# Performance work log

Hardware: AMD Instinct MI355X
Metric: run time of the kernel (lower is better)

The kernel has to match this reference:

```python
import jax, jax.numpy as jnp
import numpy as np

INPUT_SIZE = 1024
HIDDEN_SIZE = 1024
BATCH = 4096


def setup_inputs() -> dict:
    key = jax.random.key(0)
    ks = jax.random.split(key, 20)
    k = 1.0 / HIDDEN_SIZE
    bound = float(np.sqrt(k))

    def u(kk, shape):
        return jax.random.uniform(kk, shape, jnp.float32, -bound, bound)

    inp = {
        "x": jax.random.normal(ks[0], (BATCH, INPUT_SIZE), jnp.float32),
        "h0": jax.random.normal(ks[1], (BATCH, HIDDEN_SIZE), jnp.float32),
        "c0": jax.random.normal(ks[2], (BATCH, HIDDEN_SIZE), jnp.float32),
        "W_ii": u(ks[3], (INPUT_SIZE, HIDDEN_SIZE)), "b_ii": u(ks[4], (HIDDEN_SIZE,)),
        "W_if": u(ks[5], (INPUT_SIZE, HIDDEN_SIZE)), "b_if": u(ks[6], (HIDDEN_SIZE,)),
        "W_ig": u(ks[7], (INPUT_SIZE, HIDDEN_SIZE)), "b_ig": u(ks[8], (HIDDEN_SIZE,)),
        "W_io": u(ks[9], (INPUT_SIZE, HIDDEN_SIZE)), "b_io": u(ks[10], (HIDDEN_SIZE,)),
        "W_hi": u(ks[11], (HIDDEN_SIZE, HIDDEN_SIZE)), "b_hi": u(ks[12], (HIDDEN_SIZE,)),
        "W_hf": u(ks[13], (HIDDEN_SIZE, HIDDEN_SIZE)), "b_hf": u(ks[14], (HIDDEN_SIZE,)),
        "W_hg": u(ks[15], (HIDDEN_SIZE, HIDDEN_SIZE)), "b_hg": u(ks[16], (HIDDEN_SIZE,)),
        "W_ho": u(ks[17], (HIDDEN_SIZE, HIDDEN_SIZE)), "b_ho": u(ks[18], (HIDDEN_SIZE,)),
    }
    return inp


def reference(x, h0, c0,
              W_ii, b_ii, W_if, b_if, W_ig, b_ig, W_io, b_io,
              W_hi, b_hi, W_hf, b_hf, W_hg, b_hg, W_ho, b_ho):
    # Fuse the 4 input-side and 4 hidden-side GEMMs into two wide GEMMs,
    # then a single fused gate computation — same math as the original.
    Wi = jnp.concatenate([W_ii, W_if, W_ig, W_io], axis=1)  # [In, 4H]
    Wh = jnp.concatenate([W_hi, W_hf, W_hg, W_ho], axis=1)  # [H, 4H]
    b = jnp.concatenate([b_ii + b_hi, b_if + b_hf, b_ig + b_hg, b_io + b_ho])
    gates = x @ Wi + h0 @ Wh + b  # [B, 4H]
    zi, zf, zg, zo = jnp.split(gates, 4, axis=1)
    i = jax.nn.sigmoid(zi)
    f = jax.nn.sigmoid(zf)
    g = jnp.tanh(zg)
    o = jax.nn.sigmoid(zo)
    c1 = f * c0 + i * g
    h1 = o * c1
    return h1, c1
```

## Files before the change

### kernel.cpp

```cpp
#include <hip/hip_runtime.h>

typedef unsigned short u16;
typedef unsigned int u32;
typedef __attribute__((ext_vector_type(8))) short short8;
typedef __attribute__((ext_vector_type(4))) float f32x4;

__device__ __forceinline__ u16 f2b(float f) {
  u32 u = __builtin_bit_cast(u32, f);
  u32 r = (u + 0x7FFFu + ((u >> 16) & 1u)) >> 16;
  return (u16)r;
}

__device__ __forceinline__ void gl_lds16(const void* g, void* l) {
  __builtin_amdgcn_global_load_lds(
      (const __attribute__((address_space(1))) u32*)g,
      (__attribute__((address_space(3))) u32*)l, 16, 0, 0);
}

struct Ptrs8 { const float* p[8]; };

__global__ __launch_bounds__(256) void wt_pack(Ptrs8 w, u16* __restrict__ Wt) {
  __shared__ float lds[64 * 64];
  const int tid = threadIdx.x;
  const int bid = blockIdx.x;
  const int mat = bid >> 8;
  const int g = mat & 3, h = mat >> 2;
  const int tile = bid & 255;
  const int kt = tile >> 4, nt = tile & 15;
  const float* __restrict__ src = w.p[mat];

#pragma unroll
  for (int i = 0; i < 4; ++i) {
    int c = tid + i * 256;
    int k = c >> 4, n4 = (c & 15) * 4;
    gl_lds16(src + (size_t)(kt * 64 + k) * 1024 + nt * 64 + n4, &lds[c * 4]);
  }
  asm volatile("s_waitcnt vmcnt(0)");
  __syncthreads();

#pragma unroll
  for (int i = 0; i < 2; ++i) {
    int c = tid + i * 256;
    int n = c & 63, kb = (c >> 6) * 8;
    short8 v;
#pragma unroll
    for (int j = 0; j < 8; ++j) v[j] = (short)f2b(lds[(kb + j) * 64 + n]);
    size_t off = (size_t)(g * 1024 + nt * 64 + n) * 2048 + h * 1024 + kt * 64 + kb;
    *reinterpret_cast<short8*>(Wt + off) = v;
  }
}

__global__ __launch_bounds__(256) void xh_pack(const float* __restrict__ x,
                                               const float* __restrict__ h0,
                                               u16* __restrict__ Ap) {
  int t = blockIdx.x * 256 + threadIdx.x;
  int m = t >> 8, kc = t & 255;
  const float* src = (kc < 128) ? (x + (size_t)m * 1024 + kc * 8)
                                : (h0 + (size_t)m * 1024 + (kc - 128) * 8);
  float4 a = *reinterpret_cast<const float4*>(src);
  float4 b = *reinterpret_cast<const float4*>(src + 4);
  short8 v;
  v[0] = (short)f2b(a.x); v[1] = (short)f2b(a.y);
  v[2] = (short)f2b(a.z); v[3] = (short)f2b(a.w);
  v[4] = (short)f2b(b.x); v[5] = (short)f2b(b.y);
  v[6] = (short)f2b(b.z); v[7] = (short)f2b(b.w);
  *reinterpret_cast<short8*>(Ap + (size_t)m * 2048 + kc * 8) = v;
}

__global__ void bias_pack(Ptrs8 b, float* __restrict__ bias) {
  int i = blockIdx.x * 1024 + threadIdx.x;
  int g = i >> 10, n = i & 1023;
  bias[i] = b.p[g][n] + b.p[4 + g][n];
}

#define LD8(base, off) (*reinterpret_cast<const short8*>((base) + (off)))
#define MFMA_(a, b, c) __builtin_amdgcn_mfma_f32_16x16x32_bf16(a, b, c, 0, 0, 0)

#define READ_A(DST, BASE)                                   \
  _Pragma("unroll")                                         \
  for (int mi = 0; mi < 4; ++mi) {                          \
    DST[mi][0] = LD8(Ab, arow + (BASE + mi) * 1024 + c0k);  \
    DST[mi][1] = LD8(Ab, arow + (BASE + mi) * 1024 + c1k);  \
  }
#define READ_B(DST, GB)                                     \
  _Pragma("unroll")                                         \
  for (int g = 0; g < 2; ++g) {                             \
    DST[g][0] = LD8(Bb, bbase + (GB + g) * 4096 + c0k);     \
    DST[g][1] = LD8(Bb, bbase + (GB + g) * 4096 + c1k);     \
  }
#define MFMA_QUAD(AF, BF, MO, GO)                                              \
  __builtin_amdgcn_s_setprio(1);                                               \
  _Pragma("unroll")                                                            \
  for (int mi = 0; mi < 4; ++mi)                                               \
    _Pragma("unroll")                                                          \
    for (int g = 0; g < 2; ++g) {                                              \
      acc[MO + mi][GO + g] = MFMA_(AF[mi][0], BF[g][0], acc[MO + mi][GO + g]); \
      acc[MO + mi][GO + g] = MFMA_(AF[mi][1], BF[g][1], acc[MO + mi][GO + g]); \
    }                                                                          \
  __builtin_amdgcn_s_setprio(0);

__global__ __launch_bounds__(512, 2) void lstm_fused(
    const u16* __restrict__ Ap, const float* __restrict__ c0,
    const u16* __restrict__ Wt, const float* __restrict__ bias,
    float* __restrict__ out) {
  __shared__ u16 As[2][256 * 64];
  __shared__ u16 Bs[2][256 * 64];

  const int tid = threadIdx.x;
  const int lane = tid & 63;
  const int wid = tid >> 6;
  const int wr = wid >> 2;
  const int wc = wid & 3;
  const int fl = lane & 15;
  const int hi = lane >> 4;
  const int lo7 = fl & 7;

  const int bid0 = blockIdx.x;
  const int sbid = (bid0 & 7) * 32 + (bid0 >> 3);
  const int m0 = (sbid >> 4) * 256;
  const int n0 = (sbid & 15) * 64;

  int aoff[4], boff[4];
#pragma unroll
  for (int i = 0; i < 4; ++i) {
    const int L = tid + i * 512;
    const int r = L >> 3, cL = L & 7;
    const int cg = cL ^ (r & 7);
    aoff[i] = (m0 + r) * 2048 + cg * 8;
    const int ge = r >> 6, wce = (r >> 4) & 3, ue = r & 15;
    boff[i] = (ge * 1024 + n0 + wce * 16 + ue) * 2048 + cg * 8;
  }

  auto stageA = [&](int buf, int t, int h) {
    const int k0 = t * 64;
    gl_lds16(Ap + aoff[h] + k0, &As[buf][(tid + h * 512) * 8]);
    gl_lds16(Ap + aoff[h + 2] + k0, &As[buf][(tid + (h + 2) * 512) * 8]);
  };
  auto stageB = [&](int buf, int t, int h) {
    const int k0 = t * 64;
    gl_lds16(Wt + boff[2 * h] + k0, &Bs[buf][(tid + (2 * h) * 512) * 8]);
    gl_lds16(Wt + boff[2 * h + 1] + k0, &Bs[buf][(tid + (2 * h + 1) * 512) * 8]);
  };

  const int c0k = (hi ^ lo7) * 8;
  const int c1k = ((4 + hi) ^ lo7) * 8;
  const int arow = (wr * 128 + fl) * 64;
  const int bbase = (wc * 16 + fl) * 64;

  f32x4 acc[8][4] = {};

  stageB(0, 0, 0);
  stageA(0, 0, 0);
  stageA(0, 0, 1);
  stageB(0, 0, 1);

  for (int t = 0; t < 31; ++t) {
    const int cur = t & 1, nxt = cur ^ 1;
    const u16* Ab = &As[cur][0];
    const u16* Bb = &Bs[cur][0];
    short8 af03[4][2], af47[4][2], bf01[2][2], bf23[2][2];

    asm volatile("s_waitcnt vmcnt(4)" ::: "memory");
    __builtin_amdgcn_s_barrier();
    READ_A(af03, 0)
    READ_B(bf01, 0)
    stageB(nxt, t + 1, 0);
    MFMA_QUAD(af03, bf01, 0, 0)

    asm volatile("s_waitcnt vmcnt(4)" ::: "memory");
    __builtin_amdgcn_s_barrier();
    READ_A(af47, 4)
    stageA(nxt, t + 1, 0);
    MFMA_QUAD(af47, bf01, 4, 0)

    asm volatile("s_waitcnt vmcnt(4)" ::: "memory");
    __builtin_amdgcn_s_barrier();
    READ_B(bf23, 2)
    stageA(nxt, t + 1, 1);
    MFMA_QUAD(af03, bf23, 0, 2)

    __builtin_amdgcn_s_barrier();
    stageB(nxt, t + 1, 1);
    MFMA_QUAD(af47, bf23, 4, 2)
  }

  {
    const u16* Ab = &As[1][0];
    const u16* Bb = &Bs[1][0];
    short8 af03[4][2], af47[4][2], bf01[2][2], bf23[2][2];

    asm volatile("s_waitcnt vmcnt(4)" ::: "memory");
    __builtin_amdgcn_s_barrier();
    READ_A(af03, 0)
    READ_B(bf01, 0)
    MFMA_QUAD(af03, bf01, 0, 0)

    asm volatile("s_waitcnt vmcnt(2)" ::: "memory");
    __builtin_amdgcn_s_barrier();
    READ_A(af47, 4)
    MFMA_QUAD(af47, bf01, 4, 0)

    asm volatile("s_waitcnt vmcnt(0)" ::: "memory");
    __builtin_amdgcn_s_barrier();
    READ_B(bf23, 2)
    MFMA_QUAD(af03, bf23, 0, 2)

    __builtin_amdgcn_s_barrier();
    MFMA_QUAD(af47, bf23, 4, 2)
  }

  const int col = n0 + wc * 16 + fl;
  float bv[4];
#pragma unroll
  for (int g = 0; g < 4; ++g) bv[g] = bias[g * 1024 + col];

#pragma unroll
  for (int mi = 0; mi < 8; ++mi) {
#pragma unroll
    for (int r = 0; r < 4; ++r) {
      const int row = m0 + wr * 128 + mi * 16 + hi * 4 + r;
      const float zi = acc[mi][0][r] + bv[0];
      const float zf = acc[mi][1][r] + bv[1];
      const float zg = acc[mi][2][r] + bv[2];
      const float zo = acc[mi][3][r] + bv[3];
      const float ig = 1.f / (1.f + __expf(-zi));
      const float fg = 1.f / (1.f + __expf(-zf));
      const float gg = 1.f - 2.f / (__expf(2.f * zg) + 1.f);
      const float og = 1.f / (1.f + __expf(-zo));
      const float c0v = c0[(size_t)row * 1024 + col];
      const float c1 = fg * c0v + ig * gg;
      const float h1 = og * c1;
      out[(size_t)row * 1024 + col] = h1;
      out[(size_t)4194304 + (size_t)row * 1024 + col] = c1;
    }
  }
}

extern "C" void kernel_launch(void* const* d_in, const int* in_sizes, int n_in,
                              void* d_out, int out_size, void* d_ws, size_t ws_size,
                              hipStream_t stream) {
  const float* x  = (const float*)d_in[0];
  const float* h0 = (const float*)d_in[1];
  const float* c0 = (const float*)d_in[2];
  Ptrs8 w, b;
  for (int i = 0; i < 4; ++i) {
    w.p[i]     = (const float*)d_in[3 + 2 * i];
    b.p[i]     = (const float*)d_in[4 + 2 * i];
    w.p[4 + i] = (const float*)d_in[11 + 2 * i];
    b.p[4 + i] = (const float*)d_in[12 + 2 * i];
  }
  u16* Wt = (u16*)d_ws;
  u16* Ap = (u16*)((char*)d_ws + (size_t)4096 * 2048 * 2);
  float* bias = (float*)((char*)d_ws + (size_t)2 * 4096 * 2048 * 2);
  float* out = (float*)d_out;

  wt_pack<<<2048, 256, 0, stream>>>(w, Wt);
  xh_pack<<<4096, 256, 0, stream>>>(x, h0, Ap);
  bias_pack<<<4, 1024, 0, stream>>>(b, bias);
  lstm_fused<<<256, 512, 0, stream>>>(Ap, c0, Wt, bias, out);
}
```

Measured before the change: 91.95 us.

## Restructure GEMM main loop into ping-pong barrier schedule with explicit LDS waits

Reorders the per-iteration schedule so each phase issues LDS reads and the next-tile global-to-LDS stage, then synchronises with extra barriers and explicit lgkmcnt waits before the MFMA block. It also moves the vmcnt waits to the end of phases and puts the A stages before the B stages. The goal is to make the waves of the two co-resident workgroups alternate between memory and MFMA phases in a ping-pong pattern, so loads and math overlap better. The cost is roughly twice as many barriers per iteration, plus a risk of LDS races if the buffer ordering is wrong.

```diff
diff --git a/kernel.cpp b/kernel.cpp
--- a/kernel.cpp
+++ b/kernel.cpp
@@ -99,6 +99,9 @@
     }                                                                          \
   __builtin_amdgcn_s_setprio(0);
 
+#define BAR __builtin_amdgcn_s_barrier()
+#define LGKM0 asm volatile("s_waitcnt lgkmcnt(0)")
+
 __global__ __launch_bounds__(512, 2) void lstm_fused(
     const u16* __restrict__ Ap, const float* __restrict__ c0,
     const u16* __restrict__ Wt, const float* __restrict__ bias,
@@ -149,10 +152,12 @@
 
   f32x4 acc[8][4] = {};
 
-  stageB(0, 0, 0);
   stageA(0, 0, 0);
   stageA(0, 0, 1);
+  stageB(0, 0, 0);
   stageB(0, 0, 1);
+  asm volatile("s_waitcnt vmcnt(2)" ::: "memory");
+  BAR;
 
   for (int t = 0; t < 31; ++t) {
     const int cur = t & 1, nxt = cur ^ 1;
@@ -160,28 +165,35 @@
     const u16* Bb = &Bs[cur][0];
     short8 af03[4][2], af47[4][2], bf01[2][2], bf23[2][2];
 
-    asm volatile("s_waitcnt vmcnt(4)" ::: "memory");
-    __builtin_amdgcn_s_barrier();
     READ_A(af03, 0)
     READ_B(bf01, 0)
+    stageA(nxt, t + 1, 0);
+    asm volatile("s_waitcnt lgkmcnt(8)");
+    BAR;
+    LGKM0;
+    MFMA_QUAD(af03, bf01, 0, 0)
+    BAR;
+
+    READ_A(af47, 4)
+    stageA(nxt, t + 1, 1);
+    BAR;
+    LGKM0;
+    MFMA_QUAD(af47, bf01, 4, 0)
+    asm volatile("s_waitcnt vmcnt(4)" ::: "memory");
+    BAR;
+
+    READ_B(bf23, 2)
     stageB(nxt, t + 1, 0);
-    MFMA_QUAD(af03, bf01, 0, 0)
-
-    asm volatile("s_waitcnt vmcnt(4)" ::: "memory");
-    __builtin_amdgcn_s_barrier();
-    READ_A(af47, 4)
-    stageA(nxt, t + 1, 0);
-    MFMA_QUAD(af47, bf01, 4, 0)
-
-    asm volatile("s_waitcnt vmcnt(4)" ::: "memory");
-    __builtin_amdgcn_s_barrier();
-    READ_B(bf23, 2)
-    stageA(nxt, t + 1, 1);
+    BAR;
+    LGKM0;
     MFMA_QUAD(af03, bf23, 0, 2)
-
-    __builtin_amdgcn_s_barrier();
+    BAR;
+
     stageB(nxt, t + 1, 1);
+    BAR;
     MFMA_QUAD(af47, bf23, 4, 2)
+    asm volatile("s_waitcnt vmcnt(2)" ::: "memory");
+    BAR;
   }
 
   {
@@ -189,23 +201,26 @@
     const u16* Bb = &Bs[1][0];
     short8 af03[4][2], af47[4][2], bf01[2][2], bf23[2][2];
 
-    asm volatile("s_waitcnt vmcnt(4)" ::: "memory");
-    __builtin_amdgcn_s_barrier();
     READ_A(af03, 0)
     READ_B(bf01, 0)
+    BAR;
+    LGKM0;
     MFMA_QUAD(af03, bf01, 0, 0)
-
-    asm volatile("s_waitcnt vmcnt(2)" ::: "memory");
-    __builtin_amdgcn_s_barrier();
+    BAR;
+
     READ_A(af47, 4)
+    BAR;
+    LGKM0;
     MFMA_QUAD(af47, bf01, 4, 0)
-
     asm volatile("s_waitcnt vmcnt(0)" ::: "memory");
-    __builtin_amdgcn_s_barrier();
+    BAR;
+
     READ_B(bf23, 2)
+    BAR;
+    LGKM0;
     MFMA_QUAD(af03, bf23, 0, 2)
-
-    __builtin_amdgcn_s_barrier();
+    BAR;
+
     MFMA_QUAD(af47, bf23, 4, 2)
   }
 
```

Result: no change. 92.42 us (+0.5%).

## Simplify GEMM main loop to one barrier per k-step with bulk staging

Applied to the files above, without the earlier changes.

Replaces the four-phase interleaved main loop with a single-barrier loop. Each k-step now waits for all outstanding global-to-LDS loads, reads every A and B fragment from LDS, issues the full next-tile prefetch, then runs all MFMAs. It also drops the s_setprio raises around the MFMA groups and folds the peeled last iteration into the loop behind a guard. This cuts barrier count and scheduling complexity, but the vmcnt(0) wait exposes the full load latency each step and removes the fine-grained overlap of staging with compute.

```diff
diff --git a/kernel.cpp b/kernel.cpp
--- a/kernel.cpp
+++ b/kernel.cpp
@@ -89,15 +89,13 @@
     DST[g][1] = LD8(Bb, bbase + (GB + g) * 4096 + c1k);     \
   }
 #define MFMA_QUAD(AF, BF, MO, GO)                                              \
-  __builtin_amdgcn_s_setprio(1);                                               \
   _Pragma("unroll")                                                            \
   for (int mi = 0; mi < 4; ++mi)                                               \
     _Pragma("unroll")                                                          \
     for (int g = 0; g < 2; ++g) {                                              \
       acc[MO + mi][GO + g] = MFMA_(AF[mi][0], BF[g][0], acc[MO + mi][GO + g]); \
       acc[MO + mi][GO + g] = MFMA_(AF[mi][1], BF[g][1], acc[MO + mi][GO + g]); \
-    }                                                                          \
-  __builtin_amdgcn_s_setprio(0);
+    }
 
 __global__ __launch_bounds__(512, 2) void lstm_fused(
     const u16* __restrict__ Ap, const float* __restrict__ c0,
@@ -131,15 +129,14 @@
     boff[i] = (ge * 1024 + n0 + wce * 16 + ue) * 2048 + cg * 8;
   }
 
-  auto stageA = [&](int buf, int t, int h) {
+  auto stage = [&](int buf, int t) {
     const int k0 = t * 64;
-    gl_lds16(Ap + aoff[h] + k0, &As[buf][(tid + h * 512) * 8]);
-    gl_lds16(Ap + aoff[h + 2] + k0, &As[buf][(tid + (h + 2) * 512) * 8]);
-  };
-  auto stageB = [&](int buf, int t, int h) {
-    const int k0 = t * 64;
-    gl_lds16(Wt + boff[2 * h] + k0, &Bs[buf][(tid + (2 * h) * 512) * 8]);
-    gl_lds16(Wt + boff[2 * h + 1] + k0, &Bs[buf][(tid + (2 * h + 1) * 512) * 8]);
+#pragma unroll
+    for (int i = 0; i < 4; ++i)
+      gl_lds16(Ap + aoff[i] + k0, &As[buf][(tid + i * 512) * 8]);
+#pragma unroll
+    for (int i = 0; i < 4; ++i)
+      gl_lds16(Wt + boff[i] + k0, &Bs[buf][(tid + i * 512) * 8]);
   };
 
   const int c0k = (hi ^ lo7) * 8;
@@ -149,63 +146,27 @@
 
   f32x4 acc[8][4] = {};
 
-  stageB(0, 0, 0);
-  stageA(0, 0, 0);
-  stageA(0, 0, 1);
-  stageB(0, 0, 1);
-
-  for (int t = 0; t < 31; ++t) {
+  stage(0, 0);
+
+  for (int t = 0; t < 32; ++t) {
     const int cur = t & 1, nxt = cur ^ 1;
     const u16* Ab = &As[cur][0];
     const u16* Bb = &Bs[cur][0];
-    short8 af03[4][2], af47[4][2], bf01[2][2], bf23[2][2];
-
-    asm volatile("s_waitcnt vmcnt(4)" ::: "memory");
-    __builtin_amdgcn_s_barrier();
-    READ_A(af03, 0)
-    READ_B(bf01, 0)
-    stageB(nxt, t + 1, 0);
-    MFMA_QUAD(af03, bf01, 0, 0)
-
-    asm volatile("s_waitcnt vmcnt(4)" ::: "memory");
-    __builtin_amdgcn_s_barrier();
-    READ_A(af47, 4)
-    stageA(nxt, t + 1, 0);
-    MFMA_QUAD(af47, bf01, 4, 0)
-
-    asm volatile("s_waitcnt vmcnt(4)" ::: "memory");
-    __builtin_amdgcn_s_barrier();
-    READ_B(bf23, 2)
-    stageA(nxt, t + 1, 1);
-    MFMA_QUAD(af03, bf23, 0, 2)
-
-    __builtin_amdgcn_s_barrier();
-    stageB(nxt, t + 1, 1);
-    MFMA_QUAD(af47, bf23, 4, 2)
-  }
-
-  {
-    const u16* Ab = &As[1][0];
-    const u16* Bb = &Bs[1][0];
-    short8 af03[4][2], af47[4][2], bf01[2][2], bf23[2][2];
-
-    asm volatile("s_waitcnt vmcnt(4)" ::: "memory");
-    __builtin_amdgcn_s_barrier();
-    READ_A(af03, 0)
-    READ_B(bf01, 0)
-    MFMA_QUAD(af03, bf01, 0, 0)
-
-    asm volatile("s_waitcnt vmcnt(2)" ::: "memory");
-    __builtin_amdgcn_s_barrier();
-    READ_A(af47, 4)
-    MFMA_QUAD(af47, bf01, 4, 0)
 
     asm volatile("s_waitcnt vmcnt(0)" ::: "memory");
     __builtin_amdgcn_s_barrier();
+
+    short8 af03[4][2], af47[4][2], bf01[2][2], bf23[2][2];
+    READ_B(bf01, 0)
+    READ_A(af03, 0)
+    READ_A(af47, 4)
     READ_B(bf23, 2)
+
+    if (t < 31) stage(nxt, t + 1);
+
+    MFMA_QUAD(af03, bf01, 0, 0)
+    MFMA_QUAD(af47, bf01, 4, 0)
     MFMA_QUAD(af03, bf23, 0, 2)
-
-    __builtin_amdgcn_s_barrier();
     MFMA_QUAD(af47, bf23, 4, 2)
   }
 
```

Result: slower. 94.39 us (+2.6%).
